# Optimization experiments

Measured on AMD Instinct MI355X. Metric: run time of the kernel, lower is better.

## Reference

```python
import jax, jax.numpy as jnp
import numpy as np

CUR, FULL, BS, D = 1024, 2048, 4, 1024
HN, HD = 16, 64
PREV = FULL - CUR
SCALE = 1.0 / HD ** 0.5


def rel_shift(x):
    # x: (bs, hn, cur, full) -> TXL relative shift over last two dims
    b, h, q, k = x.shape
    x = jnp.pad(x, ((0, 0), (0, 0), (0, 0), (1, 0)))  # (b,h,q,k+1)
    x = x.reshape(b, h, k + 1, q)[:, :, 1:, :]
    return x.reshape(b, h, q, k)


def setup_inputs() -> dict:
    key = jax.random.key(0)
    ks = jax.random.split(key, 16)
    s = 0.02
    inputs = jax.random.normal(ks[0], (CUR, BS, D), jnp.float32)
    pos_embedding = jax.random.normal(ks[1], (FULL, 1, D), jnp.float32)
    full_input = jax.random.normal(ks[2], (FULL, BS, D), jnp.float32)
    # causal mask: query i (absolute pos i+PREV) cannot attend to key j > i+PREV
    i = jnp.arange(CUR)[:, None]
    j = jnp.arange(FULL)[None, :]
    mask = (j > i + PREV)[:, :, None]  # (cur, full, 1) bool
    W_kv = jax.random.normal(ks[3], (D, 2 * HN * HD), jnp.float32) * s
    b_kv = jnp.zeros((2 * HN * HD,), jnp.float32)
    W_q = jax.random.normal(ks[4], (D, HN * HD), jnp.float32) * s
    b_q = jnp.zeros((HN * HD,), jnp.float32)
    W_pos = jax.random.normal(ks[5], (D, HN * HD), jnp.float32) * s
    b_pos = jnp.zeros((HN * HD,), jnp.float32)
    W_proj = jax.random.normal(ks[6], (HN * HD, D), jnp.float32) * s
    b_proj = jnp.zeros((D,), jnp.float32)
    u = jax.random.normal(ks[7], (HN, HD), jnp.float32) * s
    v = jax.random.normal(ks[8], (HN, HD), jnp.float32) * s
    return dict(inputs=inputs, pos_embedding=pos_embedding, full_input=full_input,
                u=u, v=v, mask=mask, W_kv=W_kv, b_kv=b_kv, W_q=W_q, b_q=b_q,
                W_pos=W_pos, b_pos=b_pos, W_proj=W_proj, b_proj=b_proj)


def reference(inputs, pos_embedding, full_input, u, v, mask,
              W_kv, b_kv, W_q, b_q, W_pos, b_pos, W_proj, b_proj):
    cur, bs, _ = inputs.shape
    full = full_input.shape[0]
    kv = full_input @ W_kv + b_kv                      # (full, bs, 2*hn*hd)
    k, val = jnp.split(kv, 2, axis=-1)
    k = k.reshape(full, bs, HN, HD)
    val = val.reshape(full, bs, HN, HD)
    q = (inputs @ W_q + b_q).reshape(cur, bs, HN, HD)
    r = (pos_embedding @ W_pos + b_pos).reshape(full, HN, HD)
    content = jnp.einsum('ibhd,jbhd->bhij', q + u, k)   # (bs,hn,cur,full)
    position = jnp.einsum('ibhd,jhd->bhij', q + v, r)
    position = rel_shift(position)
    attn = (content + position) * SCALE
    attn = jnp.where(mask[None, :, :, 0][:, None, :, :], -jnp.inf, attn)
    attn = jax.nn.softmax(attn, axis=-1)
    out = jnp.einsum('bhij,jbhd->ibhd', attn, val).reshape(cur, bs, HN * HD)
    return out @ W_proj + b_proj
```

## Files before the change

### kernel.cpp

```cpp
#include <hip/hip_runtime.h>


typedef _Float16 half8 __attribute__((ext_vector_type(8)));
typedef _Float16 half4v __attribute__((ext_vector_type(4)));
typedef float f32x4 __attribute__((ext_vector_type(4)));

typedef const __attribute__((address_space(1))) void* gas_ptr;
typedef __attribute__((address_space(3))) void* las_ptr;

__device__ __forceinline__ void load_lds16(const void* g, void* l) {
  __builtin_amdgcn_global_load_lds((gas_ptr)g, (las_ptr)l, 16, 0, 0);
}

__global__ __launch_bounds__(256) void prep(
    const float* __restrict__ inputs, const float* __restrict__ full_inp,
    const float* __restrict__ pos_emb, const float* __restrict__ Wq,
    const float* __restrict__ Wkv, const float* __restrict__ Wpos,
    const float* __restrict__ Wproj, _Float16* __restrict__ o_in,
    _Float16* __restrict__ o_full, _Float16* __restrict__ o_pos,
    _Float16* __restrict__ owq, _Float16* __restrict__ owkv,
    _Float16* __restrict__ owpos, _Float16* __restrict__ owproj) {
  __shared__ _Float16 tile[64][65];
  const int bx = blockIdx.x;
  const int t = threadIdx.x;
  if (bx < 2048) {
#pragma unroll
    for (int it = 0; it < 7; ++it) {
      const size_t g = (size_t)bx * 256 + t + (size_t)it * (2048 * 256);
      float4 vv;
      _Float16* dptr;
      if (g < (1u << 20)) {
        const int rd = (int)(g >> 8), b = rd >> 10, i = rd & 1023;
        const size_t sg = ((size_t)(i * 4 + b) << 8) + (g & 255);
        vv = *(const float4*)(inputs + sg * 4);
        dptr = o_in + g * 4;
      } else if (g < (3u << 20)) {
        const size_t gd = g - (1u << 20);
        const int rd = (int)(gd >> 8), b = rd >> 11, j = rd & 2047;
        const size_t sg = ((size_t)(j * 4 + b) << 8) + (gd & 255);
        vv = *(const float4*)(full_inp + sg * 4);
        dptr = o_full + gd * 4;
      } else {
        const size_t gd = g - (3u << 20);
        vv = *(const float4*)(pos_emb + gd * 4);
        dptr = o_pos + gd * 4;
      }
      half4v hh;
      hh[0] = (_Float16)vv.x; hh[1] = (_Float16)vv.y;
      hh[2] = (_Float16)vv.z; hh[3] = (_Float16)vv.w;
      *(half4v*)dptr = hh;
    }
    return;
  }
  const int wb = bx - 2048;
  const float* W;
  _Float16* Wt;
  int N, tidx;
  if (wb < 256) { W = Wq; Wt = owq; N = 1024; tidx = wb; }
  else if (wb < 768) { W = Wkv; Wt = owkv; N = 2048; tidx = wb - 256; }
  else if (wb < 1024) { W = Wpos; Wt = owpos; N = 1024; tidx = wb - 768; }
  else { W = Wproj; Wt = owproj; N = 1024; tidx = wb - 1024; }
  const int K = 1024;
  const int n0 = (tidx % (N >> 6)) * 64, k0 = (tidx / (N >> 6)) * 64;
  const int rr = t >> 2, cc = (t & 3) * 16;
#pragma unroll
  for (int i = 0; i < 4; ++i) {
    float4 v = *(const float4*)&W[(size_t)(k0 + rr) * N + n0 + cc + i * 4];
    tile[rr][cc + i * 4 + 0] = (_Float16)v.x;
    tile[rr][cc + i * 4 + 1] = (_Float16)v.y;
    tile[rr][cc + i * 4 + 2] = (_Float16)v.z;
    tile[rr][cc + i * 4 + 3] = (_Float16)v.w;
  }
  __syncthreads();
  const int n = t >> 2, kc = (t & 3) * 16;
#pragma unroll
  for (int i = 0; i < 4; ++i) {
    half4v h;
    h[0] = tile[kc + i * 4 + 0][n];
    h[1] = tile[kc + i * 4 + 1][n];
    h[2] = tile[kc + i * 4 + 2][n];
    h[3] = tile[kc + i * 4 + 3][n];
    *(half4v*)&Wt[(size_t)(n0 + n) * K + k0 + kc + i * 4] = h;
  }
}

__global__ __launch_bounds__(256, 2) void gemm3(
    const _Float16* __restrict__ Aq, const _Float16* __restrict__ Akv,
    const _Float16* __restrict__ Ar, const _Float16* __restrict__ Btq,
    const _Float16* __restrict__ Btkv, const _Float16* __restrict__ Btr,
    const float* __restrict__ bq, const float* __restrict__ bkv,
    const float* __restrict__ br, const float* __restrict__ uu,
    _Float16* __restrict__ qfu, _Float16* __restrict__ kf,
    _Float16* __restrict__ vfT, _Float16* __restrict__ rf) {
  __shared__ _Float16 smem[128 * 128];
  _Float16* As = smem;
  _Float16* Bs = smem + 8192;
  const int gb = blockIdx.x;
  const _Float16* A;
  const _Float16* Bt;
  const float* bias;
  int mode, bm, bn;
  if (gb < 256) {
    mode = 1; A = Aq; Bt = Btq; bias = bq;
    bn = (gb & 7) * 128; bm = (gb >> 3) * 128;
  } else if (gb < 1280) {
    mode = 2; A = Akv; Bt = Btkv; bias = bkv;
    const int j = gb - 256;
    bn = (j & 15) * 128; bm = (j >> 4) * 128;
  } else {
    mode = 3; A = Ar; Bt = Btr; bias = br;
    const int j = gb - 1280;
    bn = (j & 7) * 128; bm = (j >> 3) * 128;
  }
  const int K = 1024;
  const int t = threadIdx.x, w = t >> 6, l = t & 63;
  const int l15 = l & 15, l4 = l >> 4;
  const int wm = (w >> 1) * 64, wn = (w & 1) * 64;

  f32x4 acc[4][4];
  const f32x4 z4 = {0.f, 0.f, 0.f, 0.f};
#pragma unroll
  for (int i = 0; i < 4; ++i)
#pragma unroll
    for (int j = 0; j < 4; ++j) acc[i][j] = z4;

  const char* Abase = (const char*)A + (size_t)bm * K * 2;
  const char* Bbase = (const char*)Bt + (size_t)bn * K * 2;

  for (int k0 = 0; k0 < K; k0 += 64) {
    __syncthreads();
#pragma unroll
    for (int iss = 0; iss < 4; ++iss) {
      const int off = w * 4096 + iss * 1024 + l * 16;
      const int row = off >> 7;
      const int sw = ((((off >> 4) & 7) ^ (row & 7)) << 4);
      load_lds16(Abase + (size_t)row * (K * 2) + k0 * 2 + sw, (char*)As + off);
      load_lds16(Bbase + (size_t)row * (K * 2) + k0 * 2 + sw, (char*)Bs + off);
    }
    __syncthreads();
#pragma unroll
    for (int ks = 0; ks < 2; ++ks) {
      const int ch = ((ks * 4 + l4) ^ (l15 & 7)) * 8;
      half8 af[4], bf[4];
#pragma unroll
      for (int mt = 0; mt < 4; ++mt)
        af[mt] = *(const half8*)&As[(wm + mt * 16 + l15) * 64 + ch];
#pragma unroll
      for (int nt = 0; nt < 4; ++nt)
        bf[nt] = *(const half8*)&Bs[(wn + nt * 16 + l15) * 64 + ch];
#pragma unroll
      for (int mt = 0; mt < 4; ++mt)
#pragma unroll
        for (int nt = 0; nt < 4; ++nt)
          acc[mt][nt] = __builtin_amdgcn_mfma_f32_16x16x32_f16(
              af[mt], bf[nt], acc[mt][nt], 0, 0, 0);
    }
  }

  if (mode == 2 && bn >= 1024) {
    const int b = bm >> 11, j0m = bm & 2047;
    const int hbase = (bn - 1024) >> 6;
#pragma unroll
    for (int ch = 0; ch < 2; ++ch) {
      __syncthreads();
      if (((wn >> 6) & 1) == ch) {
#pragma unroll
        for (int mt = 0; mt < 4; ++mt)
#pragma unroll
          for (int r = 0; r < 4; ++r) {
            const int rowl = wm + mt * 16 + l4 * 4 + r;
#pragma unroll
            for (int nt = 0; nt < 4; ++nt) {
              const int coll = nt * 16 + l15;
              smem[rowl * 66 + coll] =
                  (_Float16)(acc[mt][nt][r] + bias[bn + wn + coll]);
            }
          }
      }
      __syncthreads();
#pragma unroll
      for (int it = 0; it < 4; ++it) {
        const int c = t + 256 * it;
        const int d = c >> 4, ck = c & 15;
        half8 v8;
#pragma unroll
        for (int z = 0; z < 8; ++z) v8[z] = smem[(ck * 8 + z) * 66 + d];
        *(half8*)&vfT[(((size_t)(b * 16 + hbase + ch) * 64 + d) << 11) + j0m +
                      ck * 8] = v8;
      }
    }
    return;
  }

#pragma unroll
  for (int mt = 0; mt < 4; ++mt)
#pragma unroll
    for (int r = 0; r < 4; ++r) {
      const int rowl = wm + mt * 16 + l4 * 4 + r;
#pragma unroll
      for (int nt = 0; nt < 4; ++nt) {
        const int col = bn + wn + nt * 16 + l15;
        const float val = acc[mt][nt][r] + bias[col];
        if (mode == 1) {
          const int b = bm >> 10, i0m = bm & 1023;
          const int h = col >> 6, d = col & 63;
          qfu[(((size_t)(b * 16 + h) * 1024 + i0m + rowl) << 6) + d] =
              (_Float16)((val + uu[col]) * 0.125f);
        } else if (mode == 2) {
          const int b = bm >> 11, j0m = bm & 2047;
          const int h = col >> 6, d = col & 63;
          kf[(((size_t)(b * 16 + h) * 2048 + j0m + rowl) << 6) + d] =
              (_Float16)val;
        } else {
          const int h = col >> 6, d = col & 63;
          rf[(((size_t)h * 2048 + bm + rowl) << 6) + d] = (_Float16)val;
        }
      }
    }
}

__global__ __launch_bounds__(256, 2) void gemm_proj(
    const _Float16* __restrict__ A, const _Float16* __restrict__ Bt,
    const float* __restrict__ bias, float* __restrict__ out0, int M, int N,
    int K) {
  __shared__ _Float16 As[128 * 64];
  __shared__ _Float16 Bs[128 * 64];
  const int t = threadIdx.x, w = t >> 6, l = t & 63;
  const int l15 = l & 15, l4 = l >> 4;
  const int bm = blockIdx.y * 128, bn = blockIdx.x * 128;
  const int wm = (w >> 1) * 64, wn = (w & 1) * 64;

  f32x4 acc[4][4];
  const f32x4 z4 = {0.f, 0.f, 0.f, 0.f};
#pragma unroll
  for (int i = 0; i < 4; ++i)
#pragma unroll
    for (int j = 0; j < 4; ++j) acc[i][j] = z4;

  const char* Abase = (const char*)A + (size_t)bm * K * 2;
  const char* Bbase = (const char*)Bt + (size_t)bn * K * 2;

  for (int k0 = 0; k0 < K; k0 += 64) {
    __syncthreads();
#pragma unroll
    for (int iss = 0; iss < 4; ++iss) {
      const int off = w * 4096 + iss * 1024 + l * 16;
      const int row = off >> 7;
      const int sw = ((((off >> 4) & 7) ^ (row & 7)) << 4);
      load_lds16(Abase + (size_t)row * (K * 2) + k0 * 2 + sw, (char*)As + off);
      load_lds16(Bbase + (size_t)row * (K * 2) + k0 * 2 + sw, (char*)Bs + off);
    }
    __syncthreads();
#pragma unroll
    for (int ks = 0; ks < 2; ++ks) {
      const int ch = ((ks * 4 + l4) ^ (l15 & 7)) * 8;
      half8 af[4], bf[4];
#pragma unroll
      for (int mt = 0; mt < 4; ++mt)
        af[mt] = *(const half8*)&As[(wm + mt * 16 + l15) * 64 + ch];
#pragma unroll
      for (int nt = 0; nt < 4; ++nt)
        bf[nt] = *(const half8*)&Bs[(wn + nt * 16 + l15) * 64 + ch];
#pragma unroll
      for (int mt = 0; mt < 4; ++mt)
#pragma unroll
        for (int nt = 0; nt < 4; ++nt)
          acc[mt][nt] = __builtin_amdgcn_mfma_f32_16x16x32_f16(
              af[mt], bf[nt], acc[mt][nt], 0, 0, 0);
    }
  }

#pragma unroll
  for (int mt = 0; mt < 4; ++mt)
#pragma unroll
    for (int r = 0; r < 4; ++r) {
      const int row = bm + wm + mt * 16 + l4 * 4 + r;
#pragma unroll
      for (int nt = 0; nt < 4; ++nt) {
        const int col = bn + wn + nt * 16 + l15;
        out0[(size_t)row * N + col] = acc[mt][nt][r] + bias[col];
      }
    }
}

__global__ __launch_bounds__(256, 2) void attn_mfma(
    const _Float16* __restrict__ qfu,
    const _Float16* __restrict__ kf,
    const _Float16* __restrict__ vfT,
    const _Float16* __restrict__ rf,
    const float* __restrict__ u,
    const float* __restrict__ v,
    _Float16* __restrict__ attn_out)
{
  __shared__ _Float16 ks[64 * 64];
  __shared__ _Float16 vts[64 * 64];
  __shared__ _Float16 rs[256 * 64];
  __shared__ _Float16 pA[2][4][16 * 64];

  const int t = threadIdx.x, w = t >> 6, l = t & 63;
  const int l15 = l & 15, l4 = l >> 4;
  const int id = blockIdx.x;
  const int bh = ((id >> 3) & 7) * 8 + (id & 7);
  const int qt = id >> 6;
  const int bx = (qt < 4) ? (7 - qt) : (qt - 4);
  const int i0 = bx * 128;
  const int h = bh & 15, b = bh >> 4;

  const char* kfb = (const char*)(kf + (((size_t)bh * 2048) << 6));
  const char* vg = (const char*)(vfT + (((size_t)bh) << 17));
  const char* rg = (const char*)(rf + (((size_t)h) << 17));

  half8 qa0[2], qa1[2], qv0[2], qv1[2];
  {
    half8 dl0, dl1;
#pragma unroll
    for (int z = 0; z < 8; ++z) {
      const int di = l4 * 8 + z;
      dl0[z] = (_Float16)(0.125f * (v[h * 64 + di] - u[h * 64 + di]));
      dl1[z] = (_Float16)(0.125f * (v[h * 64 + 32 + di] - u[h * 64 + 32 + di]));
    }
#pragma unroll
    for (int g = 0; g < 2; ++g) {
      const size_t qo =
          (((size_t)bh * 1024 + i0 + 64 * g + w * 16 + l15) << 6) + l4 * 8;
      qa0[g] = *(const half8*)(qfu + qo);
      qa1[g] = *(const half8*)(qfu + qo + 32);
      qv0[g] = qa0[g] + dl0;
      qv1[g] = qa1[g] + dl1;
    }
  }
  const f32x4 z4 = {0.f, 0.f, 0.f, 0.f};
  f32x4 o[2][4];
  float lsum[2][4];
#pragma unroll
  for (int g = 0; g < 2; ++g)
#pragma unroll
    for (int nt = 0; nt < 4; ++nt) { o[g][nt] = z4; lsum[g][nt] = 0.f; }

  const int mb0 = 960 - i0;
  const int njt = 2 * bx + 18;

#pragma unroll
  for (int iss = 0; iss < 6; ++iss) {
    const int off = w * 1024 + iss * 4096 + l * 16;
    const int q = off >> 7;
    const int cph = (off >> 4) & 7;
    const int slot = (mb0 - 64 + q) & 255;
    int m = mb0 - 64 + q;
    m = m < 2047 ? m : 2047;
    load_lds16(rg + (size_t)m * 128 + ((cph ^ (slot & 7)) << 4),
               (char*)rs + slot * 128 + cph * 16);
  }

  for (int jt = 0; jt < njt; ++jt) {
    const int j0 = jt * 64;
    const int m_base = j0 - i0 + 960;
    __syncthreads();
    {
      const char* kg = kfb + (size_t)j0 * 128;
#pragma unroll
      for (int iss = 0; iss < 2; ++iss) {
        const int off = w * 1024 + iss * 4096 + l * 16;
        const int row = off >> 7;
        const int cph = (off >> 4) & 7;
        const int sw = ((cph ^ (row & 7)) << 4);
        load_lds16(kg + (size_t)row * 128 + sw, (char*)ks + off);
        load_lds16(vg + (size_t)row * 4096 + (size_t)j0 * 2 + sw,
                   (char*)vts + off);
      }
    }
    if (jt > 0) {
      const int m0 = m_base + 64;
#pragma unroll
      for (int iss = 0; iss < 2; ++iss) {
        const int off = w * 1024 + iss * 4096 + l * 16;
        const int q = off >> 7;
        const int cph = (off >> 4) & 7;
        const int slot = (m0 + q) & 255;
        int m = m0 + q;
        m = m < 2047 ? m : 2047;
        load_lds16(rg + (size_t)m * 128 + ((cph ^ (slot & 7)) << 4),
                   (char*)rs + slot * 128 + cph * 16);
      }
    }
    __syncthreads();

    f32x4 sc[2][4];
#pragma unroll
    for (int nt = 0; nt < 4; ++nt) {
      const int row = nt * 16 + l15;
      const int rsw = row & 7;
      const half8 b0 = *(const half8*)&ks[row * 64 + ((l4 ^ rsw) * 8)];
      const half8 b1 = *(const half8*)&ks[row * 64 + (((4 + l4) ^ rsw) * 8)];
#pragma unroll
      for (int g = 0; g < 2; ++g) {
        f32x4 cc = z4;
        cc = __builtin_amdgcn_mfma_f32_16x16x32_f16(qa0[g], b0, cc, 0, 0, 0);
        cc = __builtin_amdgcn_mfma_f32_16x16x32_f16(qa1[g], b1, cc, 0, 0, 0);
        sc[g][nt] = cc;
      }
    }

#pragma unroll
    for (int g = 0; g < 2; ++g) {
      const int cw = i0 + 64 * g - j0 + 1024 + 16 * w;
      if (g == 0 && cw < -15) continue;
      const int mbg = m_base - 64 * g;
      f32x4 accP[5];
#pragma unroll
      for (int p = 0; p < 5; ++p) {
        const int m = mbg + (3 - w + p) * 16 + l15;
        const int slot = m & 255;
        const int ssw = slot & 7;
        const half8 b0 = *(const half8*)&rs[slot * 64 + ((l4 ^ ssw) * 8)];
        const half8 b1 = *(const half8*)&rs[slot * 64 + (((4 + l4) ^ ssw) * 8)];
        f32x4 cc = z4;
        cc = __builtin_amdgcn_mfma_f32_16x16x32_f16(qv0[g], b0, cc, 0, 0, 0);
        cc = __builtin_amdgcn_mfma_f32_16x16x32_f16(qv1[g], b1, cc, 0, 0, 0);
        accP[p] = cc;
      }
      if (cw >= 63) {
#pragma unroll
        for (int r = 0; r < 4; ++r) {
          const int thr = 4 * l4 + r;
          const int srcl = (l4 << 4) | ((15 + l15 - thr) & 15);
          float rot[5];
#pragma unroll
          for (int p = 0; p < 5; ++p) rot[p] = __shfl(accP[p][r], srcl, 64);
          float esum = 0.f;
          const int sw2 = (thr & 7) * 8;
#pragma unroll
          for (int nt = 0; nt < 4; ++nt) {
            const float pv = (l15 <= thr) ? rot[nt] : rot[nt + 1];
            const float e = __expf(sc[g][nt][r] + pv);
            esum += e;
            pA[g][w][thr * 64 + ((16 * nt + l15) ^ sw2)] = (_Float16)e;
          }
          lsum[g][r] += esum;
        }
      } else {
#pragma unroll
        for (int r = 0; r < 4; ++r) {
          const int thr = 4 * l4 + r;
          const int srcl = (l4 << 4) | ((15 + l15 - thr) & 15);
          float rot[5];
#pragma unroll
          for (int p = 0; p < 5; ++p) rot[p] = __shfl(accP[p][r], srcl, 64);
          float esum = 0.f;
          const int sw2 = (thr & 7) * 8;
#pragma unroll
          for (int nt = 0; nt < 4; ++nt) {
            const float pv = (l15 <= thr) ? rot[nt] : rot[nt + 1];
            const bool masked = (16 * nt + l15) > (cw + thr);
            const float e = masked ? 0.f : __expf(sc[g][nt][r] + pv);
            esum += e;
            pA[g][w][thr * 64 + ((16 * nt + l15) ^ sw2)] = (_Float16)e;
          }
          lsum[g][r] += esum;
        }
      }
    }

    const bool act0 = (i0 - j0 + 1024 + 16 * w) >= -15;
#pragma unroll
    for (int kk = 0; kk < 2; ++kk) {
      const int aoff = l15 * 64 + ((kk * 32 + l4 * 8) ^ ((l15 & 7) * 8));
      half8 a81 = *(const half8*)&pA[1][w][aoff];
      half8 a80;
      if (act0) a80 = *(const half8*)&pA[0][w][aoff];
#pragma unroll
      for (int nt = 0; nt < 4; ++nt) {
        const int row = nt * 16 + l15;
        const half8 b8 =
            *(const half8*)&vts[row * 64 + ((((kk << 2) + l4) ^ (row & 7)) * 8)];
        if (act0)
          o[0][nt] =
              __builtin_amdgcn_mfma_f32_16x16x32_f16(a80, b8, o[0][nt], 0, 0, 0);
        o[1][nt] =
            __builtin_amdgcn_mfma_f32_16x16x32_f16(a81, b8, o[1][nt], 0, 0, 0);
      }
    }
  }

#pragma unroll
  for (int g = 0; g < 2; ++g)
#pragma unroll
    for (int r = 0; r < 4; ++r) {
      float s = lsum[g][r];
      s += __shfl_xor(s, 1, 64);
      s += __shfl_xor(s, 2, 64);
      s += __shfl_xor(s, 4, 64);
      s += __shfl_xor(s, 8, 64);
      const float inv = 1.0f / s;
      const int i = i0 + 64 * g + w * 16 + l4 * 4 + r;
      const size_t base = ((size_t)i * 4 + b) * 1024 + h * 64;
#pragma unroll
      for (int nt = 0; nt < 4; ++nt)
        attn_out[base + nt * 16 + l15] = (_Float16)(o[g][nt][r] * inv);
    }
}

extern "C" void kernel_launch(void* const* d_in, const int* in_sizes, int n_in,
                              void* d_out, int out_size, void* d_ws,
                              size_t ws_size, hipStream_t stream) {
  const float* inputs   = (const float*)d_in[0];
  const float* pos_emb  = (const float*)d_in[1];
  const float* full_inp = (const float*)d_in[2];
  const float* u        = (const float*)d_in[3];
  const float* v        = (const float*)d_in[4];
  const float* W_kv   = (const float*)d_in[6];
  const float* b_kv   = (const float*)d_in[7];
  const float* W_q    = (const float*)d_in[8];
  const float* b_q    = (const float*)d_in[9];
  const float* W_pos  = (const float*)d_in[10];
  const float* b_pos  = (const float*)d_in[11];
  const float* W_proj = (const float*)d_in[12];
  const float* b_proj = (const float*)d_in[13];
  float* out = (float*)d_out;

  char* ws = (char*)d_ws;
  const size_t MB = 1024 * 1024;
  _Float16* in_q_h    = (_Float16*)(ws);
  _Float16* in_full_h = (_Float16*)(ws + 8 * MB);
  _Float16* in_pos_h  = (_Float16*)(ws + 24 * MB);
  _Float16* attn_h    = (_Float16*)(ws + 28 * MB);
  _Float16* wq_t      = (_Float16*)(ws + 36 * MB);
  _Float16* wkv_t     = (_Float16*)(ws + 38 * MB);
  _Float16* wpos_t    = (_Float16*)(ws + 42 * MB);
  _Float16* wproj_t   = (_Float16*)(ws + 44 * MB);
  _Float16* qfu       = (_Float16*)(ws + 46 * MB);
  _Float16* kf        = (_Float16*)(ws + 54 * MB);
  _Float16* vfT       = (_Float16*)(ws + 70 * MB);
  _Float16* rf        = (_Float16*)(ws + 86 * MB);

  const dim3 blk(256);
  prep<<<dim3(3328), blk, 0, stream>>>(inputs, full_inp, pos_emb, W_q, W_kv,
                                       W_pos, W_proj, in_q_h, in_full_h,
                                       in_pos_h, wq_t, wkv_t, wpos_t, wproj_t);
  gemm3<<<dim3(1408), blk, 0, stream>>>(in_q_h, in_full_h, in_pos_h, wq_t,
                                        wkv_t, wpos_t, b_q, b_kv, b_pos, u,
                                        qfu, kf, vfT, rf);
  attn_mfma<<<dim3(512), blk, 0, stream>>>(qfu, kf, vfT, rf, u, v, attn_h);
  gemm_proj<<<dim3(8, 32), blk, 0, stream>>>(attn_h, wproj_t, b_proj, out,
                                             4096, 1024, 1024);
}
```

Baseline: 335.0 us.

## Load positional R rows directly from global into registers, drop LDS ring buffer

Removes the 256-row shared-memory ring buffer for the positional projection R and its async global-to-LDS prefetches. Each wave now loads its R fragments straight from global memory (L2-resident, shared across batches) into registers, and the loop is restructured to handle the two query groups one after another so the second group's R loads can overlap the first group's softmax. This cuts LDS use by 32 KB, which may raise occupancy, and removes LDS traffic. The cost is more global/L2 loads, since each wave reloads overlapping R rows, and higher register pressure. The g=0 R fragments are also now loaded and multiplied even when that group is fully masked.

```diff
diff --git a/kernel.cpp b/kernel.cpp
--- a/kernel.cpp
+++ b/kernel.cpp
@@ -294,7 +294,6 @@
 {
   __shared__ _Float16 ks[64 * 64];
   __shared__ _Float16 vts[64 * 64];
-  __shared__ _Float16 rs[256 * 64];
   __shared__ _Float16 pA[2][4][16 * 64];
 
   const int t = threadIdx.x, w = t >> 6, l = t & 63;
@@ -308,7 +307,7 @@
 
   const char* kfb = (const char*)(kf + (((size_t)bh * 2048) << 6));
   const char* vg = (const char*)(vfT + (((size_t)bh) << 17));
-  const char* rg = (const char*)(rf + (((size_t)h) << 17));
+  const _Float16* rg = rf + (((size_t)h) << 17);
 
   half8 qa0[2], qa1[2], qv0[2], qv1[2];
   {
@@ -337,20 +336,7 @@
 #pragma unroll
     for (int nt = 0; nt < 4; ++nt) { o[g][nt] = z4; lsum[g][nt] = 0.f; }
 
-  const int mb0 = 960 - i0;
   const int njt = 2 * bx + 18;
-
-#pragma unroll
-  for (int iss = 0; iss < 6; ++iss) {
-    const int off = w * 1024 + iss * 4096 + l * 16;
-    const int q = off >> 7;
-    const int cph = (off >> 4) & 7;
-    const int slot = (mb0 - 64 + q) & 255;
-    int m = mb0 - 64 + q;
-    m = m < 2047 ? m : 2047;
-    load_lds16(rg + (size_t)m * 128 + ((cph ^ (slot & 7)) << 4),
-               (char*)rs + slot * 128 + cph * 16);
-  }
 
   for (int jt = 0; jt < njt; ++jt) {
     const int j0 = jt * 64;
@@ -369,56 +355,52 @@
                    (char*)vts + off);
       }
     }
-    if (jt > 0) {
-      const int m0 = m_base + 64;
-#pragma unroll
-      for (int iss = 0; iss < 2; ++iss) {
-        const int off = w * 1024 + iss * 4096 + l * 16;
-        const int q = off >> 7;
-        const int cph = (off >> 4) & 7;
-        const int slot = (m0 + q) & 255;
-        int m = m0 + q;
-        m = m < 2047 ? m : 2047;
-        load_lds16(rg + (size_t)m * 128 + ((cph ^ (slot & 7)) << 4),
-                   (char*)rs + slot * 128 + cph * 16);
-      }
-    }
     __syncthreads();
 
-    f32x4 sc[2][4];
+    const int cw0 = i0 - j0 + 1024 + 16 * w;
+    const bool act0 = cw0 >= -15;
+
+    half8 rb0[5][2];
+#pragma unroll
+    for (int p = 0; p < 5; ++p) {
+      int m = m_base + (3 - w + p) * 16 + l15;
+      m = m < 2047 ? m : 2047;
+      const half8* rrow = (const half8*)(rg + ((size_t)m << 6));
+      rb0[p][0] = rrow[l4];
+      rb0[p][1] = rrow[4 + l4];
+    }
+
+    f32x4 sc[4];
 #pragma unroll
     for (int nt = 0; nt < 4; ++nt) {
       const int row = nt * 16 + l15;
       const int rsw = row & 7;
       const half8 b0 = *(const half8*)&ks[row * 64 + ((l4 ^ rsw) * 8)];
       const half8 b1 = *(const half8*)&ks[row * 64 + (((4 + l4) ^ rsw) * 8)];
-#pragma unroll
-      for (int g = 0; g < 2; ++g) {
-        f32x4 cc = z4;
-        cc = __builtin_amdgcn_mfma_f32_16x16x32_f16(qa0[g], b0, cc, 0, 0, 0);
-        cc = __builtin_amdgcn_mfma_f32_16x16x32_f16(qa1[g], b1, cc, 0, 0, 0);
-        sc[g][nt] = cc;
-      }
-    }
-
-#pragma unroll
-    for (int g = 0; g < 2; ++g) {
-      const int cw = i0 + 64 * g - j0 + 1024 + 16 * w;
-      if (g == 0 && cw < -15) continue;
-      const int mbg = m_base - 64 * g;
-      f32x4 accP[5];
-#pragma unroll
-      for (int p = 0; p < 5; ++p) {
-        const int m = mbg + (3 - w + p) * 16 + l15;
-        const int slot = m & 255;
-        const int ssw = slot & 7;
-        const half8 b0 = *(const half8*)&rs[slot * 64 + ((l4 ^ ssw) * 8)];
-        const half8 b1 = *(const half8*)&rs[slot * 64 + (((4 + l4) ^ ssw) * 8)];
-        f32x4 cc = z4;
-        cc = __builtin_amdgcn_mfma_f32_16x16x32_f16(qv0[g], b0, cc, 0, 0, 0);
-        cc = __builtin_amdgcn_mfma_f32_16x16x32_f16(qv1[g], b1, cc, 0, 0, 0);
-        accP[p] = cc;
-      }
+      f32x4 cc = z4;
+      cc = __builtin_amdgcn_mfma_f32_16x16x32_f16(qa0[0], b0, cc, 0, 0, 0);
+      cc = __builtin_amdgcn_mfma_f32_16x16x32_f16(qa1[0], b1, cc, 0, 0, 0);
+      sc[nt] = cc;
+    }
+    f32x4 accP[5];
+#pragma unroll
+    for (int p = 0; p < 5; ++p) {
+      f32x4 cc = z4;
+      cc = __builtin_amdgcn_mfma_f32_16x16x32_f16(qv0[0], rb0[p][0], cc, 0, 0, 0);
+      cc = __builtin_amdgcn_mfma_f32_16x16x32_f16(qv1[0], rb0[p][1], cc, 0, 0, 0);
+      accP[p] = cc;
+    }
+    half8 rb1[5][2];
+#pragma unroll
+    for (int p = 0; p < 5; ++p) {
+      int m = m_base - 64 + (3 - w + p) * 16 + l15;
+      m = m < 2047 ? m : 2047;
+      const half8* rrow = (const half8*)(rg + ((size_t)m << 6));
+      rb1[p][0] = rrow[l4];
+      rb1[p][1] = rrow[4 + l4];
+    }
+    if (act0) {
+      const int cw = cw0;
       if (cw >= 63) {
 #pragma unroll
         for (int r = 0; r < 4; ++r) {
@@ -432,11 +414,11 @@
 #pragma unroll
           for (int nt = 0; nt < 4; ++nt) {
             const float pv = (l15 <= thr) ? rot[nt] : rot[nt + 1];
-            const float e = __expf(sc[g][nt][r] + pv);
+            const float e = __expf(sc[nt][r] + pv);
             esum += e;
-            pA[g][w][thr * 64 + ((16 * nt + l15) ^ sw2)] = (_Float16)e;
+            pA[0][w][thr * 64 + ((16 * nt + l15) ^ sw2)] = (_Float16)e;
           }
-          lsum[g][r] += esum;
+          lsum[0][r] += esum;
         }
       } else {
 #pragma unroll
@@ -452,16 +434,76 @@
           for (int nt = 0; nt < 4; ++nt) {
             const float pv = (l15 <= thr) ? rot[nt] : rot[nt + 1];
             const bool masked = (16 * nt + l15) > (cw + thr);
-            const float e = masked ? 0.f : __expf(sc[g][nt][r] + pv);
+            const float e = masked ? 0.f : __expf(sc[nt][r] + pv);
             esum += e;
-            pA[g][w][thr * 64 + ((16 * nt + l15) ^ sw2)] = (_Float16)e;
+            pA[0][w][thr * 64 + ((16 * nt + l15) ^ sw2)] = (_Float16)e;
           }
-          lsum[g][r] += esum;
+          lsum[0][r] += esum;
         }
       }
     }
-
-    const bool act0 = (i0 - j0 + 1024 + 16 * w) >= -15;
+#pragma unroll
+    for (int nt = 0; nt < 4; ++nt) {
+      const int row = nt * 16 + l15;
+      const int rsw = row & 7;
+      const half8 b0 = *(const half8*)&ks[row * 64 + ((l4 ^ rsw) * 8)];
+      const half8 b1 = *(const half8*)&ks[row * 64 + (((4 + l4) ^ rsw) * 8)];
+      f32x4 cc = z4;
+      cc = __builtin_amdgcn_mfma_f32_16x16x32_f16(qa0[1], b0, cc, 0, 0, 0);
+      cc = __builtin_amdgcn_mfma_f32_16x16x32_f16(qa1[1], b1, cc, 0, 0, 0);
+      sc[nt] = cc;
+    }
+#pragma unroll
+    for (int p = 0; p < 5; ++p) {
+      f32x4 cc = z4;
+      cc = __builtin_amdgcn_mfma_f32_16x16x32_f16(qv0[1], rb1[p][0], cc, 0, 0, 0);
+      cc = __builtin_amdgcn_mfma_f32_16x16x32_f16(qv1[1], rb1[p][1], cc, 0, 0, 0);
+      accP[p] = cc;
+    }
+    {
+      const int cw = cw0 + 64;
+      if (cw >= 63) {
+#pragma unroll
+        for (int r = 0; r < 4; ++r) {
+          const int thr = 4 * l4 + r;
+          const int srcl = (l4 << 4) | ((15 + l15 - thr) & 15);
+          float rot[5];
+#pragma unroll
+          for (int p = 0; p < 5; ++p) rot[p] = __shfl(accP[p][r], srcl, 64);
+          float esum = 0.f;
+          const int sw2 = (thr & 7) * 8;
+#pragma unroll
+          for (int nt = 0; nt < 4; ++nt) {
+            const float pv = (l15 <= thr) ? rot[nt] : rot[nt + 1];
+            const float e = __expf(sc[nt][r] + pv);
+            esum += e;
+            pA[1][w][thr * 64 + ((16 * nt + l15) ^ sw2)] = (_Float16)e;
+          }
+          lsum[1][r] += esum;
+        }
+      } else {
+#pragma unroll
+        for (int r = 0; r < 4; ++r) {
+          const int thr = 4 * l4 + r;
+          const int srcl = (l4 << 4) | ((15 + l15 - thr) & 15);
+          float rot[5];
+#pragma unroll
+          for (int p = 0; p < 5; ++p) rot[p] = __shfl(accP[p][r], srcl, 64);
+          float esum = 0.f;
+          const int sw2 = (thr & 7) * 8;
+#pragma unroll
+          for (int nt = 0; nt < 4; ++nt) {
+            const float pv = (l15 <= thr) ? rot[nt] : rot[nt + 1];
+            const bool masked = (16 * nt + l15) > (cw + thr);
+            const float e = masked ? 0.f : __expf(sc[nt][r] + pv);
+            esum += e;
+            pA[1][w][thr * 64 + ((16 * nt + l15) ^ sw2)] = (_Float16)e;
+          }
+          lsum[1][r] += esum;
+        }
+      }
+    }
+
 #pragma unroll
     for (int kk = 0; kk < 2; ++kk) {
       const int aoff = l15 * 64 + ((kk * 32 + l4 * 8) ^ ((l15 & 7) * 8));
```

Measured after the change: 381.7 us. 1.14x slower.
